# Optimization experiments

Measured on AMD Instinct MI355X. Metric: run time of the kernel, lower is better.

## Reference

```python
import jax, jax.numpy as jnp
import numpy as np

N_BUS = 2048


def setup_inputs() -> dict:
    key = jax.random.key(0)
    ks = jax.random.split(key, 16)
    n_x, n_rbf, n_bus, batch = 4096, 1024, N_BUS, 8192
    s = lambda fan_in: 1.0 / np.sqrt(fan_in)
    return {
        "x": jax.random.normal(ks[0], (batch, n_x), dtype=jnp.float32),
        "W_h": jax.random.uniform(ks[1], (n_rbf, n_x), jnp.float32, -s(n_x), s(n_x)),
        "b_h": jax.random.uniform(ks[2], (n_rbf,), jnp.float32, -s(n_x), s(n_x)),
        "W_h2": jax.random.uniform(ks[3], (n_rbf, n_rbf), jnp.float32, -s(n_rbf), s(n_rbf)),
        "b_h2": jax.random.uniform(ks[4], (n_rbf,), jnp.float32, -s(n_rbf), s(n_rbf)),
        "W_y": jax.random.uniform(ks[5], (2 * n_bus, n_rbf), jnp.float32, -s(n_rbf), s(n_rbf)),
        "b_y": jax.random.uniform(ks[6], (2 * n_bus,), jnp.float32, -s(n_rbf), s(n_rbf)),
        "G": jax.random.uniform(ks[7], (n_bus, n_bus), dtype=jnp.float32),
        "Bm": jax.random.uniform(ks[8], (n_bus, n_bus), dtype=jnp.float32),
        "bias_p": jnp.zeros((1, n_bus), jnp.float32),
        "bias_q": jnp.zeros((1, n_bus), jnp.float32),
        "W_p": jax.random.uniform(ks[9], (n_bus, n_bus), jnp.float32, -s(n_bus), s(n_bus)),
        "b_p": jax.random.uniform(ks[10], (n_bus,), jnp.float32, -s(n_bus), s(n_bus)),
        "W_q": jax.random.uniform(ks[11], (n_bus, n_bus), jnp.float32, -s(n_bus), s(n_bus)),
        "b_q": jax.random.uniform(ks[12], (n_bus,), jnp.float32, -s(n_bus), s(n_bus)),
    }


def reference(x, W_h, b_h, W_h2, b_h2, W_y, b_y, G, Bm, bias_p, bias_q, W_p, b_p, W_q, b_q):
    n_bus = N_BUS
    # encoder (intended math: ReLU activations)
    h1 = jax.nn.relu(x @ W_h.T + b_h)
    h2 = jax.nn.relu(h1 @ W_h2.T + b_h2)
    uw = h2 @ W_y.T + b_y                     # [B, 2*n_bus]
    u, w = uw[:, :n_bus], uw[:, n_bus:]
    # decoder: algebraically identical to summing the masked outer products over dim 2:
    # p_i = sum_k (u_i u_k + w_i w_k) G_ik + (w_i u_k - u_i w_k) B_ik
    #     = u_i (G u)_i + w_i (G w)_i + w_i (B u)_i - u_i (B w)_i
    Gu = u @ G.T
    Gw = w @ G.T
    Bu = u @ Bm.T
    Bw = w @ Bm.T
    p = u * Gu + w * Gw + w * Bu - u * Bw + bias_p
    q = w * Gu - u * Gw - u * Bu - w * Bw + bias_q
    p = p @ W_p.T + b_p
    q = q @ W_q.T + b_q
    return (uw, p, q)
```

## Files before the change

### kernel.cpp

```cpp
#include <hip/hip_runtime.h>

typedef __bf16 bf16;
typedef __bf16 bf16x8 __attribute__((ext_vector_type(8)));
typedef __bf16 bf16x4 __attribute__((ext_vector_type(4)));
typedef float  f32x4  __attribute__((ext_vector_type(4)));

__device__ __forceinline__ void async_load16(const void* g, void* l) {
    __builtin_amdgcn_global_load_lds(
        (const __attribute__((address_space(1))) void*)g,
        (__attribute__((address_space(3))) void*)l,
        16, 0, 0);
}

__global__ __launch_bounds__(256) void cast_f32_bf16(
        const float* __restrict__ s, bf16* __restrict__ d, int n) {
    int i = (blockIdx.x * 256 + threadIdx.x) * 8;
    if (i >= n) return;
    f32x4 v0 = *(const f32x4*)(s + i);
    f32x4 v1 = *(const f32x4*)(s + i + 4);
    bf16x8 o;
    o[0] = (bf16)v0[0]; o[1] = (bf16)v0[1]; o[2] = (bf16)v0[2]; o[3] = (bf16)v0[3];
    o[4] = (bf16)v1[0]; o[5] = (bf16)v1[1]; o[6] = (bf16)v1[2]; o[7] = (bf16)v1[3];
    *(bf16x8*)(d + i) = o;
}

__global__ __launch_bounds__(256) void fill_f32(float* p, float v, int n) {
    int i = blockIdx.x * 256 + threadIdx.x;
    if (i < n) p[i] = v;
}

template<int RELU, int WF32, int WBF16>
__global__ __launch_bounds__(256, 3) void gemm_bt(
        const bf16* __restrict__ A, int lda,
        const bf16* __restrict__ B, int ldb,
        const float* __restrict__ bias,
        float* __restrict__ Cf, int ldcf,
        bf16* __restrict__ Cb, int ldcb,
        int M, int N, int K) {
    (void)M; (void)N;
    __shared__ __attribute__((aligned(16))) bf16 lA[128 * 32];
    __shared__ __attribute__((aligned(16))) bf16 lB[128 * 32];

    const int t = threadIdx.x;
    const int w = t >> 6, lane = t & 63;
    const int wm = w >> 1, wn = w & 1;
    const int m0 = blockIdx.y * 128, n0 = blockIdx.x * 128;
    const int lane15 = lane & 15, quad = lane >> 4;

    f32x4 acc[4][4] = {};

    const int srow = lane >> 2;
    const int scol = (lane & 3) * 8;
    const int c0 = 2 * w, c1 = 2 * w + 1;
    const bf16* gA0 = A + (size_t)(m0 + c0 * 16 + srow) * lda + scol;
    const bf16* gA1 = A + (size_t)(m0 + c1 * 16 + srow) * lda + scol;
    const bf16* gB0 = B + (size_t)(n0 + c0 * 16 + srow) * ldb + scol;
    const bf16* gB1 = B + (size_t)(n0 + c1 * 16 + srow) * ldb + scol;
    bf16* lA0 = &lA[c0 * 512];
    bf16* lA1 = &lA[c1 * 512];
    bf16* lB0 = &lB[c0 * 512];
    bf16* lB1 = &lB[c1 * 512];

    const bf16* fA = &lA[(wm * 64 + lane15) * 32 + quad * 8];
    const bf16* fB = &lB[(wn * 64 + lane15) * 32 + quad * 8];

    for (int k0 = 0; k0 < K; k0 += 32) {
        async_load16(gA0, lA0);
        async_load16(gA1, lA1);
        async_load16(gB0, lB0);
        async_load16(gB1, lB1);
        gA0 += 32; gA1 += 32; gB0 += 32; gB1 += 32;
        __syncthreads();
        bf16x8 a[4], b[4];
#pragma unroll
        for (int i = 0; i < 4; i++) a[i] = *(const bf16x8*)(fA + i * 16 * 32);
#pragma unroll
        for (int j = 0; j < 4; j++) b[j] = *(const bf16x8*)(fB + j * 16 * 32);
#pragma unroll
        for (int i = 0; i < 4; i++)
#pragma unroll
            for (int j = 0; j < 4; j++)
                acc[i][j] = __builtin_amdgcn_mfma_f32_16x16x32_bf16(a[i], b[j], acc[i][j], 0, 0, 0);
        __syncthreads();
    }

#pragma unroll
    for (int i = 0; i < 4; i++) {
        int row = m0 + wm * 64 + i * 16 + quad * 4;
#pragma unroll
        for (int j = 0; j < 4; j++) {
            int col = n0 + wn * 64 + j * 16 + lane15;
            float bv = bias ? bias[col] : 0.0f;
#pragma unroll
            for (int r = 0; r < 4; r++) {
                float v = acc[i][j][r] + bv;
                if (RELU) v = v > 0.0f ? v : 0.0f;
                if (WF32)  Cf[(size_t)(row + r) * ldcf + col] = v;
                if (WBF16) Cb[(size_t)(row + r) * ldcb + col] = (bf16)v;
            }
        }
    }
}

__global__ __launch_bounds__(256) void combine_pq(
        const bf16* __restrict__ uwb,
        const bf16* __restrict__ GBu, const bf16* __restrict__ GBw,
        const float* __restrict__ bias_p, const float* __restrict__ bias_q,
        bf16* __restrict__ pp, bf16* __restrict__ qp) {
    int idx = (blockIdx.x * 256 + threadIdx.x) * 4;
    int row = idx >> 11;
    int col = idx & 2047;
    size_t base = (size_t)row * 4096 + col;
    bf16x4 u4  = *(const bf16x4*)(uwb + base);
    bf16x4 w4  = *(const bf16x4*)(uwb + base + 2048);
    bf16x4 gu4 = *(const bf16x4*)(GBu + base);
    bf16x4 bu4 = *(const bf16x4*)(GBu + base + 2048);
    bf16x4 gw4 = *(const bf16x4*)(GBw + base);
    bf16x4 bw4 = *(const bf16x4*)(GBw + base + 2048);
    bf16x4 po, qo;
#pragma unroll
    for (int r = 0; r < 4; r++) {
        float u = (float)u4[r], w = (float)w4[r];
        float gu = (float)gu4[r], gw = (float)gw4[r];
        float bu = (float)bu4[r], bw = (float)bw4[r];
        float p = u * gu + w * gw + w * bu - u * bw + bias_p[col + r];
        float q = w * gu - u * gw - u * bu - w * bw + bias_q[col + r];
        po[r] = (bf16)p;
        qo[r] = (bf16)q;
    }
    *(bf16x4*)(pp + idx) = po;
    *(bf16x4*)(qp + idx) = qo;
}

extern "C" void kernel_launch(void* const* d_in, const int* in_sizes, int n_in,
                              void* d_out, int out_size, void* d_ws, size_t ws_size,
                              hipStream_t stream) {
    (void)in_sizes; (void)n_in;
    const int BT = 8192, NX = 4096, NR = 1024, NB = 2048;

    const float* x      = (const float*)d_in[0];
    const float* W_h    = (const float*)d_in[1];
    const float* b_h    = (const float*)d_in[2];
    const float* W_h2   = (const float*)d_in[3];
    const float* b_h2   = (const float*)d_in[4];
    const float* W_y    = (const float*)d_in[5];
    const float* b_y    = (const float*)d_in[6];
    const float* G      = (const float*)d_in[7];
    const float* Bm     = (const float*)d_in[8];
    const float* bias_p = (const float*)d_in[9];
    const float* bias_q = (const float*)d_in[10];
    const float* W_p    = (const float*)d_in[11];
    const float* b_p    = (const float*)d_in[12];
    const float* W_q    = (const float*)d_in[13];
    const float* b_q    = (const float*)d_in[14];
    float* out = (float*)d_out;

    const size_t NEED = 320864256ull;
    if (ws_size < NEED) {
        fill_f32<<<dim3((out_size + 255) / 256), dim3(256), 0, stream>>>(
            out, (float)(ws_size >> 20), out_size);
        return;
    }
    char* ws = (char*)d_ws;
    bf16* xb   = (bf16*)(ws + 0);
    bf16* GBu  = (bf16*)(ws + 0);
    bf16* uwb  = (bf16*)(ws + 67108864);
    bf16* GBw  = (bf16*)(ws + 134217728);
    bf16* h1   = (bf16*)(ws + 201326592);
    bf16* pp   = (bf16*)(ws + 201326592);
    bf16* h2   = (bf16*)(ws + 218103808);
    bf16* qp   = (bf16*)(ws + 234881024);
    bf16* whb  = (bf16*)(ws + 268435456);
    bf16* wh2b = (bf16*)(ws + 276824064);
    bf16* wyb  = (bf16*)(ws + 278921216);
    bf16* gbm  = (bf16*)(ws + 287309824);
    bf16* wpb  = (bf16*)(ws + 304087040);
    bf16* wqb  = (bf16*)(ws + 312475648);

    dim3 blk(256);
    auto cast = [&](const float* s, bf16* d, int n) {
        cast_f32_bf16<<<dim3((n / 8 + 255) / 256), blk, 0, stream>>>(s, d, n);
    };
    cast(x,    xb,   BT * NX);
    cast(W_h,  whb,  NR * NX);
    cast(W_h2, wh2b, NR * NR);
    cast(W_y,  wyb,  NX * NR);
    cast(G,    gbm,            NB * NB);
    cast(Bm,   gbm + (size_t)NB * NB, NB * NB);
    cast(W_p,  wpb,  NB * NB);
    cast(W_q,  wqb,  NB * NB);

    gemm_bt<1, 0, 1><<<dim3(NR / 128, BT / 128), blk, 0, stream>>>(
        xb, NX, whb, NX, b_h, nullptr, 0, h1, NR, BT, NR, NX);
    gemm_bt<1, 0, 1><<<dim3(NR / 128, BT / 128), blk, 0, stream>>>(
        h1, NR, wh2b, NR, b_h2, nullptr, 0, h2, NR, BT, NR, NR);
    gemm_bt<0, 1, 1><<<dim3(NX / 128, BT / 128), blk, 0, stream>>>(
        h2, NR, wyb, NR, b_y, out, NX, uwb, NX, BT, NX, NR);
    gemm_bt<0, 0, 1><<<dim3(NX / 128, BT / 128), blk, 0, stream>>>(
        uwb,      NX, gbm, NB, nullptr, nullptr, 0, GBu, NX, BT, NX, NB);
    gemm_bt<0, 0, 1><<<dim3(NX / 128, BT / 128), blk, 0, stream>>>(
        uwb + NB, NX, gbm, NB, nullptr, nullptr, 0, GBw, NX, BT, NX, NB);
    combine_pq<<<dim3(BT * NB / 4 / 256), blk, 0, stream>>>(
        uwb, GBu, GBw, bias_p, bias_q, pp, qp);
    gemm_bt<0, 1, 0><<<dim3(NB / 128, BT / 128), blk, 0, stream>>>(
        pp, NB, wpb, NB, b_p, out + (size_t)BT * NX, NB, nullptr, 0, BT, NB, NB);
    gemm_bt<0, 1, 0><<<dim3(NB / 128, BT / 128), blk, 0, stream>>>(
        qp, NB, wqb, NB, b_q, out + (size_t)BT * NX + (size_t)BT * NB, NB, nullptr, 0, BT, NB, NB);
}
```

Baseline: 1.198 ms.

## Add 256x256 double-buffered swizzled GEMM kernel for large decoder GEMMs

Adds a new GEMM kernel with 256x256 output tiles, 512 threads, K-step 64, XOR-swizzled LDS layout, double-buffered async global-to-LDS prefetch interleaved with MFMA phases, s_setprio around MFMA blocks, and an XCD-aware workgroup remapping. It replaces the 128x128 kernel for the uw, G/B, and W_p/W_q GEMMs to raise data reuse per tile and overlap loads with compute. The cost is 128KB of LDS per block, which limits occupancy, and more complex manual barrier and waitcnt scheduling that is harder to get right.

```diff
diff --git a/kernel.cpp b/kernel.cpp
--- a/kernel.cpp
+++ b/kernel.cpp
@@ -1,4 +1,5 @@
 #include <hip/hip_runtime.h>
+#include <stdint.h>
 
 typedef __bf16 bf16;
 typedef __bf16 bf16x8 __attribute__((ext_vector_type(8)));
@@ -90,6 +91,142 @@
 #pragma unroll
         for (int j = 0; j < 4; j++) {
             int col = n0 + wn * 64 + j * 16 + lane15;
+            float bv = bias ? bias[col] : 0.0f;
+#pragma unroll
+            for (int r = 0; r < 4; r++) {
+                float v = acc[i][j][r] + bv;
+                if (RELU) v = v > 0.0f ? v : 0.0f;
+                if (WF32)  Cf[(size_t)(row + r) * ldcf + col] = v;
+                if (WBF16) Cb[(size_t)(row + r) * ldcb + col] = (bf16)v;
+            }
+        }
+    }
+}
+
+template<int RELU, int WF32, int WBF16>
+__global__ __launch_bounds__(512, 2) void gemm256(
+        const bf16* __restrict__ A, int lda,
+        const bf16* __restrict__ B, int ldb,
+        const float* __restrict__ bias,
+        float* __restrict__ Cf, int ldcf,
+        bf16* __restrict__ Cb, int ldcb,
+        int K) {
+    __shared__ __attribute__((aligned(128))) char sm[131072];
+
+    const int t = threadIdx.x;
+    const int w = t >> 6;
+    const int lane = t & 63;
+    const int wm = w >> 2, wn = w & 3;
+    const int l15 = lane & 15, quad = lane >> 4;
+
+    const int gx = gridDim.x;
+    const int nwg = gx * gridDim.y;
+    const int orig = blockIdx.y * gx + blockIdx.x;
+    const int cpx = nwg >> 3;
+    const int wg = (orig & 7) * cpx + (orig >> 3);
+    const int m0 = (wg / gx) << 8;
+    const int n0 = (wg % gx) << 8;
+
+    f32x4 acc[8][4] = {};
+
+    const int srow = t >> 3;
+    const int scol = ((t & 7) ^ (srow & 7)) << 3;
+    const bf16* gA = A + (size_t)(m0 + srow) * lda + scol;
+    const bf16* gB = B + (size_t)(n0 + srow) * ldb + scol;
+    char* smA = sm + w * 1024;
+    char* smB = sm + 65536 + w * 1024;
+    const size_t stepA = (size_t)lda << 6;
+    const size_t stepB = (size_t)ldb << 6;
+
+    const int swz = (quad ^ (l15 & 7)) << 4;
+    const char* aRd0 = sm + ((wm * 128 + l15) << 7) + swz;
+    const char* bRd0 = sm + 65536 + ((wn * 64 + l15) << 7) + swz;
+    const char* aRd1 = (const char*)((uintptr_t)aRd0 ^ 64);
+    const char* bRd1 = (const char*)((uintptr_t)bRd0 ^ 64);
+
+    bf16x8 a[4][2], b[4][2];
+    unsigned boff = 0;
+
+#define STAGE_A(nb) do { \
+    async_load16(gA,             smA + (nb)); \
+    async_load16(gA + stepA,     smA + (nb) + 8192); \
+    async_load16(gA + 2 * stepA, smA + (nb) + 16384); \
+    async_load16(gA + 3 * stepA, smA + (nb) + 24576); } while (0)
+#define STAGE_B(nb) do { \
+    async_load16(gB,             smB + (nb)); \
+    async_load16(gB + stepB,     smB + (nb) + 8192); \
+    async_load16(gB + 2 * stepB, smB + (nb) + 16384); \
+    async_load16(gB + 3 * stepB, smB + (nb) + 24576); } while (0)
+#define RD_A(Mq) do { _Pragma("unroll") \
+    for (int i = 0; i < 4; i++) { \
+        a[i][0] = *(const bf16x8*)(aRd0 + boff + (Mq) * 8192 + i * 2048); \
+        a[i][1] = *(const bf16x8*)(aRd1 + boff + (Mq) * 8192 + i * 2048); } } while (0)
+#define RD_B(Nq) do { _Pragma("unroll") \
+    for (int j = 0; j < 2; j++) { \
+        b[(Nq) * 2 + j][0] = *(const bf16x8*)(bRd0 + boff + ((Nq) * 2 + j) * 2048); \
+        b[(Nq) * 2 + j][1] = *(const bf16x8*)(bRd1 + boff + ((Nq) * 2 + j) * 2048); } } while (0)
+#define MMA(Mq, Nq) do { _Pragma("unroll") \
+    for (int i = 0; i < 4; i++) { _Pragma("unroll") \
+        for (int j = 0; j < 2; j++) { \
+            acc[(Mq) * 4 + i][(Nq) * 2 + j] = __builtin_amdgcn_mfma_f32_16x16x32_bf16( \
+                a[i][0], b[(Nq) * 2 + j][0], acc[(Mq) * 4 + i][(Nq) * 2 + j], 0, 0, 0); \
+            acc[(Mq) * 4 + i][(Nq) * 2 + j] = __builtin_amdgcn_mfma_f32_16x16x32_bf16( \
+                a[i][1], b[(Nq) * 2 + j][1], acc[(Mq) * 4 + i][(Nq) * 2 + j], 0, 0, 0); } } } while (0)
+#define BAR() __builtin_amdgcn_s_barrier()
+#define WAITLGKM() do { \
+    asm volatile("s_waitcnt lgkmcnt(0)" ::: "memory"); \
+    __builtin_amdgcn_sched_barrier(0); } while (0)
+
+    STAGE_A(0); STAGE_B(0);
+    gA += 64; gB += 64;
+    asm volatile("s_waitcnt vmcnt(0)" ::: "memory");
+    BAR();
+
+    const int nt = K >> 6;
+#define KTILE(PF) do { \
+    const unsigned nboff = boff ^ 32768u; \
+     \
+    RD_A(0); RD_B(0); \
+    if (PF) STAGE_A(nboff); \
+    BAR(); WAITLGKM(); \
+    __builtin_amdgcn_s_setprio(1); MMA(0, 0); __builtin_amdgcn_s_setprio(0); \
+    BAR(); \
+     \
+    RD_B(1); \
+    if (PF) STAGE_B(nboff); \
+    BAR(); WAITLGKM(); \
+    __builtin_amdgcn_s_setprio(1); MMA(0, 1); __builtin_amdgcn_s_setprio(0); \
+    BAR(); \
+     \
+    RD_A(1); \
+    BAR(); WAITLGKM(); \
+    __builtin_amdgcn_s_setprio(1); MMA(1, 0); __builtin_amdgcn_s_setprio(0); \
+    BAR(); \
+     \
+    __builtin_amdgcn_s_setprio(1); MMA(1, 1); __builtin_amdgcn_s_setprio(0); \
+    if (PF) { gA += 64; gB += 64; \
+        asm volatile("s_waitcnt vmcnt(0)" ::: "memory"); } \
+    BAR(); \
+    boff = nboff; \
+} while (0)
+
+    for (int T = 0; T < nt - 1; ++T) KTILE(1);
+    KTILE(0);
+#undef KTILE
+#undef STAGE_A
+#undef STAGE_B
+#undef RD_A
+#undef RD_B
+#undef MMA
+#undef BAR
+#undef WAITLGKM
+
+#pragma unroll
+    for (int i = 0; i < 8; i++) {
+        int row = m0 + wm * 128 + i * 16 + quad * 4;
+#pragma unroll
+        for (int j = 0; j < 4; j++) {
+            int col = n0 + wn * 64 + j * 16 + l15;
             float bv = bias ? bias[col] : 0.0f;
 #pragma unroll
             for (int r = 0; r < 4; r++) {
@@ -194,16 +331,17 @@
         xb, NX, whb, NX, b_h, nullptr, 0, h1, NR, BT, NR, NX);
     gemm_bt<1, 0, 1><<<dim3(NR / 128, BT / 128), blk, 0, stream>>>(
         h1, NR, wh2b, NR, b_h2, nullptr, 0, h2, NR, BT, NR, NR);
-    gemm_bt<0, 1, 1><<<dim3(NX / 128, BT / 128), blk, 0, stream>>>(
-        h2, NR, wyb, NR, b_y, out, NX, uwb, NX, BT, NX, NR);
-    gemm_bt<0, 0, 1><<<dim3(NX / 128, BT / 128), blk, 0, stream>>>(
-        uwb,      NX, gbm, NB, nullptr, nullptr, 0, GBu, NX, BT, NX, NB);
-    gemm_bt<0, 0, 1><<<dim3(NX / 128, BT / 128), blk, 0, stream>>>(
-        uwb + NB, NX, gbm, NB, nullptr, nullptr, 0, GBw, NX, BT, NX, NB);
+
+    gemm256<0, 1, 1><<<dim3(NX / 256, BT / 256), dim3(512), 0, stream>>>(
+        h2, NR, wyb, NR, b_y, out, NX, uwb, NX, NR);
+    gemm256<0, 0, 1><<<dim3(NX / 256, BT / 256), dim3(512), 0, stream>>>(
+        uwb,      NX, gbm, NB, nullptr, nullptr, 0, GBu, NX, NB);
+    gemm256<0, 0, 1><<<dim3(NX / 256, BT / 256), dim3(512), 0, stream>>>(
+        uwb + NB, NX, gbm, NB, nullptr, nullptr, 0, GBw, NX, NB);
     combine_pq<<<dim3(BT * NB / 4 / 256), blk, 0, stream>>>(
         uwb, GBu, GBw, bias_p, bias_q, pp, qp);
-    gemm_bt<0, 1, 0><<<dim3(NB / 128, BT / 128), blk, 0, stream>>>(
-        pp, NB, wpb, NB, b_p, out + (size_t)BT * NX, NB, nullptr, 0, BT, NB, NB);
-    gemm_bt<0, 1, 0><<<dim3(NB / 128, BT / 128), blk, 0, stream>>>(
-        qp, NB, wqb, NB, b_q, out + (size_t)BT * NX + (size_t)BT * NB, NB, nullptr, 0, BT, NB, NB);
-}
+    gemm256<0, 1, 0><<<dim3(NB / 256, BT / 256), dim3(512), 0, stream>>>(
+        pp, NB, wpb, NB, b_p, out + (size_t)BT * NX, NB, nullptr, 0, NB);
+    gemm256<0, 1, 0><<<dim3(NB / 256, BT / 256), dim3(512), 0, stream>>>(
+        qp, NB, wqb, NB, b_q, out + (size_t)BT * NX + (size_t)BT * NB, NB, nullptr, 0, NB);
+}
```

Result: slower. 1.326 ms (+10.7%).
